# Kernel optimization log

Measured on AMD Instinct MI355X. Metric: run time of the kernel, lower is better.

## Reference

```python
import jax, jax.numpy as jnp
import numpy as np
import math

B, SQ, SK, D_MODEL, OUT_DIM = 8, 2048, 2048, 1024, 128
MASK_VALUE = -1e6  # torch code fills masked scores with -1000000.0, not -inf


def setup_inputs() -> dict:
    key = jax.random.key(0)
    ks = jax.random.split(key, 10)
    scale = 1.0 / math.sqrt(D_MODEL)
    return {
        "queries": jax.random.normal(ks[0], (B, SQ, D_MODEL), dtype=jnp.float32),
        "keys": jax.random.normal(ks[1], (B, SK, D_MODEL), dtype=jnp.float32),
        "values": jax.random.normal(ks[2], (B, SK, D_MODEL), dtype=jnp.float32),
        "valid_lens": jax.random.randint(ks[3], (B,), 1, SK + 1, dtype=jnp.int32),
        "w_q": jax.random.normal(ks[4], (D_MODEL, OUT_DIM), dtype=jnp.float32) * scale,
        "b_q": jnp.zeros((OUT_DIM,), dtype=jnp.float32),
        "w_k": jax.random.normal(ks[5], (D_MODEL, OUT_DIM), dtype=jnp.float32) * scale,
        "b_k": jnp.zeros((OUT_DIM,), dtype=jnp.float32),
        "w_v": jax.random.normal(ks[6], (D_MODEL, OUT_DIM), dtype=jnp.float32) * scale,
        "b_v": jnp.zeros((OUT_DIM,), dtype=jnp.float32),
    }


def reference(queries, keys, values, valid_lens, w_q, b_q, w_k, b_k, w_v, b_v):
    # QKV projections (LazyLinear equivalents)
    Q = queries @ w_q + b_q   # [B, SQ, OUT_DIM]
    K = keys @ w_k + b_k      # [B, SK, OUT_DIM]
    V = values @ w_v + b_v    # [B, SK, OUT_DIM]
    dim = Q.shape[-1]
    scores = jnp.einsum("bqd,bkd->bqk", Q, K) / jnp.sqrt(jnp.asarray(dim, Q.dtype))
    # masked_softmax: valid_lens [B] -> mask positions >= valid_len on the key axis
    mask = jnp.arange(scores.shape[-1])[None, None, :] < valid_lens[:, None, None]
    scores = jnp.where(mask, scores, jnp.asarray(MASK_VALUE, scores.dtype))
    attn = jax.nn.softmax(scores, axis=-1)
    return jnp.einsum("bqk,bkd->bqd", attn, V)  # [B, SQ, OUT_DIM]
```

## Files before the change

### kernel.cpp

```cpp
#include <hip/hip_runtime.h>
#include <math.h>

constexpr int BATCH  = 8;
constexpr int SEQQ   = 2048;
constexpr int SEQK   = 2048;
constexpr int DMODEL = 1024;
constexpr int ODIM   = 128;

typedef __attribute__((ext_vector_type(8))) short bf16x8;
typedef __attribute__((ext_vector_type(4))) float f32x4;

__device__ inline unsigned short f2bf(float f) {
    union { float f; unsigned int u; } v; v.f = f;
    unsigned int r = v.u + 0x7FFFu + ((v.u >> 16) & 1u);
    return (unsigned short)(r >> 16);
}

__device__ __forceinline__ unsigned int pk2bf(float a, float b) {
    unsigned int ua = __float_as_uint(a) + 0x8000u;
    unsigned int ub = __float_as_uint(b) + 0x8000u;
    return __builtin_amdgcn_perm(ub, ua, 0x07060302u);
}

__device__ __forceinline__ void gl_lds16(const void* g, void* l) {
    __builtin_amdgcn_global_load_lds(
        (const __attribute__((address_space(1))) unsigned int*)g,
        (__attribute__((address_space(3))) unsigned int*)l, 16, 0, 0);
}

__global__ __launch_bounds__(256)
void wtrans_kernel(const float* __restrict__ Wq, const float* __restrict__ Wk,
                   const float* __restrict__ Wv, unsigned short* __restrict__ Wt)
{
    const int which = blockIdx.z;
    const float* __restrict__ W = which == 0 ? Wq : (which == 1 ? Wk : Wv);
    unsigned short* __restrict__ dst = Wt + (size_t)which * DMODEL * ODIM;
    const int k0 = blockIdx.x * 32, n0 = blockIdx.y * 32;
    __shared__ unsigned short T[32][36];
    const int t = threadIdx.x;
    const int r = t >> 3, c = (t & 7) * 4;
    float4 w = *(const float4*)(W + (size_t)(k0 + r) * ODIM + n0 + c);
    T[r][c + 0] = f2bf(w.x); T[r][c + 1] = f2bf(w.y);
    T[r][c + 2] = f2bf(w.z); T[r][c + 3] = f2bf(w.w);
    __syncthreads();
    const int n = t >> 3, k4 = (t & 7) * 4;
    ushort4 o;
    o.x = T[k4 + 0][n]; o.y = T[k4 + 1][n];
    o.z = T[k4 + 2][n]; o.w = T[k4 + 3][n];
    *(ushort4*)(dst + (size_t)(n0 + n) * DMODEL + k0 + k4) = o;
}

__global__ __launch_bounds__(256, 6)
void proj_kernel(const float* __restrict__ Aq, const float* __restrict__ Ak,
                 const float* __restrict__ Av,
                 const unsigned short* __restrict__ Wt_all,
                 const float* __restrict__ bq, const float* __restrict__ bk,
                 const float* __restrict__ bv,
                 unsigned short* __restrict__ Qb, unsigned short* __restrict__ Kb,
                 unsigned short* __restrict__ Vt)
{
    const int which = blockIdx.y;
    const float* __restrict__ A    = which == 0 ? Aq : (which == 1 ? Ak : Av);
    const float* __restrict__ bias = which == 0 ? bq : (which == 1 ? bk : bv);
    const unsigned short* __restrict__ Wt = Wt_all + (size_t)which * DMODEL * ODIM;

    const int row0 = blockIdx.x * 32;
    const int t = threadIdx.x, wave = t >> 6, lane = t & 63;
    const int lrow = lane & 15, quad = lane >> 4;
    const int mh = (wave & 1) * 16;
    const int nh = (wave >> 1) * 64;

    __shared__ __align__(16) float          As[32 * 64];
    __shared__ __align__(16) unsigned short Ws[128 * 64];

    f32x4 acc[4];
#pragma unroll
    for (int nt = 0; nt < 4; ++nt)
#pragma unroll
        for (int i = 0; i < 4; ++i) acc[nt][i] = 0.f;

    const float* agp[2]; float* aldst[2];
    const unsigned short* wgp[4]; unsigned short* wldst[4];
#pragma unroll
    for (int j = 0; j < 2; ++j) {
        const int s = j * 256 + t;
        const int ar = s >> 4, ac = (s & 15) ^ (ar & 15);
        agp[j]   = A + (size_t)(row0 + ar) * DMODEL + ac * 4;
        aldst[j] = &As[s * 4];
    }
#pragma unroll
    for (int j = 0; j < 4; ++j) {
        const int s = j * 256 + t;
        const int wr = s >> 3, wc = (s & 7) ^ (wr & 7);
        wgp[j]   = Wt + (size_t)wr * DMODEL + wc * 8;
        wldst[j] = &Ws[s * 8];
    }

    const int R = mh + lrow;
    const int x4 = lrow;
    const int x3 = lrow & 7;

    for (int k0 = 0; k0 < DMODEL; k0 += 64) {
#pragma unroll
        for (int j = 0; j < 2; ++j) gl_lds16(agp[j] + k0, aldst[j]);
#pragma unroll
        for (int j = 0; j < 4; ++j) gl_lds16(wgp[j] + k0, wldst[j]);
        __syncthreads();
#pragma unroll
        for (int ks = 0; ks < 2; ++ks) {
            const int c0 = ks * 8 + quad * 2;
            float4 a0 = *(const float4*)&As[(R * 16 + (c0 ^ x4)) * 4];
            float4 a1 = *(const float4*)&As[(R * 16 + ((c0 + 1) ^ x4)) * 4];
            bf16x8 af;
            ((unsigned int*)&af)[0] = pk2bf(a0.x, a0.y);
            ((unsigned int*)&af)[1] = pk2bf(a0.z, a0.w);
            ((unsigned int*)&af)[2] = pk2bf(a1.x, a1.y);
            ((unsigned int*)&af)[3] = pk2bf(a1.z, a1.w);
#pragma unroll
            for (int nt = 0; nt < 4; ++nt) {
                const int n = nh + nt * 16 + lrow;
                const int c = (ks * 4 + quad) ^ x3;
                bf16x8 wf = *(const bf16x8*)&Ws[(n * 8 + c) * 8];
                acc[nt] = __builtin_amdgcn_mfma_f32_16x16x32_bf16(af, wf, acc[nt], 0, 0, 0);
            }
        }
        __syncthreads();
    }

    const float sc = (which == 0) ? 0.08838834764831845f : 1.0f;
    float bv_[4];
#pragma unroll
    for (int nt = 0; nt < 4; ++nt) bv_[nt] = bias[nh + nt * 16 + lrow];

    const int b  = row0 >> 11;
    const int mb = row0 & 2047;

    if (which == 2) {
#pragma unroll
        for (int nt = 0; nt < 4; ++nt) {
            const int n = nh + nt * 16 + lrow;
            ushort4 o;
            o.x = f2bf(acc[nt][0] + bv_[nt]);
            o.y = f2bf(acc[nt][1] + bv_[nt]);
            o.z = f2bf(acc[nt][2] + bv_[nt]);
            o.w = f2bf(acc[nt][3] + bv_[nt]);
            *(ushort4*)(Vt + ((size_t)b * ODIM + n) * SEQK + mb + mh + quad * 4) = o;
        }
    } else {
        unsigned short* __restrict__ Ob = (which == 0) ? Qb : Kb;
#pragma unroll
        for (int nt = 0; nt < 4; ++nt)
#pragma unroll
            for (int r = 0; r < 4; ++r) {
                float val = sc * (acc[nt][r] + bv_[nt]);
                Ob[(size_t)(row0 + mh + quad * 4 + r) * ODIM + nh + nt * 16 + lrow]
                    = f2bf(val);
            }
    }
}

__global__ __launch_bounds__(256, 3)
void flash_kernel(const unsigned short* __restrict__ Qb,
                  const unsigned short* __restrict__ Kb,
                  const unsigned short* __restrict__ Vt,
                  const int* __restrict__ valid_lens,
                  float* __restrict__ Op, float* __restrict__ Lp, int nsplit)
{
    const int b = blockIdx.y, s = blockIdx.z, q0 = blockIdx.x * 64;
    const int skh = SEQK / nsplit;
    const int t = threadIdx.x, wave = t >> 6, lane = t & 63;
    const int lrow = lane & 15, quad = lane >> 4;

    const int valid = valid_lens[b];
    const int vloc  = min(valid - s * skh, skh);

    float* __restrict__ lpart = Lp + (size_t)(s * BATCH + b) * SEQQ + q0;
    float* __restrict__ opart = Op + ((size_t)(s * BATCH + b) * SEQQ + q0) * ODIM;

    if (vloc <= 0) {
        if (t < 64) lpart[t] = 0.f;
        return;
    }

    __shared__ __align__(16) unsigned short Ks[64 * 128];
    __shared__ __align__(16) unsigned short Vs[128 * 64];
    __shared__ __align__(16) unsigned short Ps[4][16][72];

    bf16x8 qf[4];
    {
        const unsigned short* qp =
            Qb + ((size_t)b * SEQQ + q0 + wave * 16 + lrow) * ODIM + quad * 8;
#pragma unroll
        for (int ks = 0; ks < 4; ++ks) qf[ks] = *(const bf16x8*)(qp + ks * 32);
    }

    f32x4 o[8];
#pragma unroll
    for (int nt = 0; nt < 8; ++nt)
#pragma unroll
        for (int i = 0; i < 4; ++i) o[nt][i] = 0.f;
    float lsum[4] = {0.f, 0.f, 0.f, 0.f};

    const unsigned short* kgp[4]; unsigned short* kldst[4];
    const unsigned short* vgp[4]; unsigned short* vldst[4];
    const unsigned short* kbase = Kb + ((size_t)b * SEQK + s * skh) * ODIM;
    const unsigned short* vbase = Vt + (size_t)b * ODIM * SEQK + s * skh;
#pragma unroll
    for (int j = 0; j < 4; ++j) {
        const int sl = j * 256 + t;
        const int kr = sl >> 4, kc = (sl & 15) ^ (kr & 15);
        kgp[j]   = kbase + (size_t)kr * ODIM + kc * 8;
        kldst[j] = &Ks[sl * 8];
        const int vr = sl >> 3, vc = (sl & 7) ^ (vr & 7);
        vgp[j]   = vbase + (size_t)vr * SEQK + vc * 8;
        vldst[j] = &Vs[sl * 8];
    }

    const int x4 = lrow, x3 = lrow & 7;
    const int nch = (vloc + 63) >> 6;

    for (int c = 0; c < nch; ++c) {
        const int k0 = c * 64;
#pragma unroll
        for (int j = 0; j < 4; ++j) {
            gl_lds16(kgp[j] + (size_t)k0 * ODIM, kldst[j]);
            gl_lds16(vgp[j] + k0, vldst[j]);
        }
        __syncthreads();

        f32x4 sv[4];
#pragma unroll
        for (int nt = 0; nt < 4; ++nt)
#pragma unroll
            for (int i = 0; i < 4; ++i) sv[nt][i] = 0.f;
#pragma unroll
        for (int ks = 0; ks < 4; ++ks)
#pragma unroll
            for (int nt = 0; nt < 4; ++nt) {
                const int kr = nt * 16 + lrow;
                const int cc = (ks * 4 + quad) ^ x4;
                bf16x8 kf = *(const bf16x8*)&Ks[(kr * 16 + cc) * 8];
                sv[nt] = __builtin_amdgcn_mfma_f32_16x16x32_bf16(qf[ks], kf, sv[nt], 0, 0, 0);
            }

        if (k0 + 64 > vloc) {
#pragma unroll
            for (int nt = 0; nt < 4; ++nt)
                if (k0 + nt * 16 + lrow >= vloc) {
#pragma unroll
                    for (int i = 0; i < 4; ++i) sv[nt][i] = -1e30f;
                }
        }

#pragma unroll
        for (int nt = 0; nt < 4; ++nt)
#pragma unroll
            for (int r = 0; r < 4; ++r) {
                float p = __expf(sv[nt][r]);
                lsum[r] += p;
                Ps[wave][quad * 4 + r][nt * 16 + lrow] =
                    (unsigned short)((__float_as_uint(p) + 0x8000u) >> 16);
            }

        bf16x8 pf0 = *(const bf16x8*)&Ps[wave][lrow][quad * 8];
        bf16x8 pf1 = *(const bf16x8*)&Ps[wave][lrow][32 + quad * 8];

#pragma unroll
        for (int nt = 0; nt < 8; ++nt) {
            const int vrow = nt * 16 + lrow;
            bf16x8 v0 = *(const bf16x8*)&Vs[(vrow * 8 + (quad ^ x3)) * 8];
            o[nt] = __builtin_amdgcn_mfma_f32_16x16x32_bf16(pf0, v0, o[nt], 0, 0, 0);
        }
#pragma unroll
        for (int nt = 0; nt < 8; ++nt) {
            const int vrow = nt * 16 + lrow;
            bf16x8 v1 = *(const bf16x8*)&Vs[(vrow * 8 + ((4 + quad) ^ x3)) * 8];
            o[nt] = __builtin_amdgcn_mfma_f32_16x16x32_bf16(pf1, v1, o[nt], 0, 0, 0);
        }
        __syncthreads();
    }

#pragma unroll
    for (int msk = 1; msk < 16; msk <<= 1)
#pragma unroll
        for (int r = 0; r < 4; ++r) lsum[r] += __shfl_xor(lsum[r], msk);
    if (lrow == 0) {
#pragma unroll
        for (int r = 0; r < 4; ++r)
            lpart[wave * 16 + quad * 4 + r] = lsum[r];
    }

#pragma unroll
    for (int nt = 0; nt < 8; ++nt)
#pragma unroll
        for (int r = 0; r < 4; ++r)
            opart[(size_t)(wave * 16 + quad * 4 + r) * ODIM + nt * 16 + lrow]
                = o[nt][r];
}

__global__ __launch_bounds__(256)
void combine_kernel(const float* __restrict__ Op, const float* __restrict__ Lp,
                    float* __restrict__ out, int nsplit)
{
    const int idx = blockIdx.x * 256 + threadIdx.x;
    const int row = idx >> 5;
    const size_t SL = (size_t)BATCH * SEQQ;
    float l = 0.f;
    float4 acc = {0.f, 0.f, 0.f, 0.f};
    for (int s = 0; s < nsplit; ++s) {
        float ls = Lp[(size_t)s * SL + row];
        if (ls > 0.f) {
            float4 v = ((const float4*)(Op + (size_t)s * SL * ODIM))[idx];
            acc.x += v.x; acc.y += v.y; acc.z += v.z; acc.w += v.w;
            l += ls;
        }
    }
    const float inv = 1.f / l;
    float4 r;
    r.x = acc.x * inv; r.y = acc.y * inv; r.z = acc.z * inv; r.w = acc.w * inv;
    ((float4*)out)[idx] = r;
}

extern "C" void kernel_launch(void* const* d_in, const int* in_sizes, int n_in,
                              void* d_out, int out_size, void* d_ws, size_t ws_size,
                              hipStream_t stream)
{
    const float* queries    = (const float*)d_in[0];
    const float* keys       = (const float*)d_in[1];
    const float* values     = (const float*)d_in[2];
    const int*   valid_lens = (const int*)d_in[3];
    const float* w_q        = (const float*)d_in[4];
    const float* b_q        = (const float*)d_in[5];
    const float* w_k        = (const float*)d_in[6];
    const float* b_k        = (const float*)d_in[7];
    const float* w_v        = (const float*)d_in[8];
    const float* b_v        = (const float*)d_in[9];
    float* out = (float*)d_out;

    const size_t nQKV = (size_t)BATCH * SEQQ * ODIM;
    unsigned short* Qb = (unsigned short*)d_ws;
    unsigned short* Kb = Qb + nQKV;
    unsigned short* Vt = Kb + nQKV;
    unsigned short* Wt = Vt + nQKV;
    const size_t base = 3 * nQKV * sizeof(unsigned short)
                      + (size_t)3 * DMODEL * ODIM * sizeof(unsigned short);

    int KS = 4;
    if (ws_size < base + 4 * (nQKV * 4 + (size_t)BATCH * SEQQ * 4)) KS = 2;

    float* Op = (float*)((char*)d_ws + base);
    float* Lp = Op + (size_t)KS * nQKV;

    wtrans_kernel<<<dim3(DMODEL / 32, ODIM / 32, 3), 256, 0, stream>>>(w_q, w_k, w_v, Wt);

    proj_kernel<<<dim3((BATCH * SEQQ) / 32, 3), 256, 0, stream>>>(
        queries, keys, values, Wt, b_q, b_k, b_v, Qb, Kb, Vt);

    flash_kernel<<<dim3(SEQQ / 64, BATCH, KS), 256, 0, stream>>>(
        Qb, Kb, Vt, valid_lens, Op, Lp, KS);

    combine_kernel<<<(BATCH * SEQQ * ODIM / 4) / 256, 256, 0, stream>>>(Op, Lp, out, KS);
}
```

Baseline: 259.1 us.

## Double-buffer projection GEMM with register-staged A and larger row tile

The projection kernel now computes 64 rows per block instead of 32, with each wave owning a 32x64 output tile, so every W fragment read from LDS feeds two MFMAs. A is loaded into registers, converted to bf16 once and written to a swizzled bf16 LDS buffer. A and W are double-buffered so the next k-slice loads overlap the current MFMAs, which removes one barrier per iteration. This costs more LDS and registers: launch bounds drop to 3 blocks per SM and the grid is halved.

```diff
diff --git a/kernel.cpp b/kernel.cpp
--- a/kernel.cpp
+++ b/kernel.cpp
@@ -50,7 +50,7 @@
     *(ushort4*)(dst + (size_t)(n0 + n) * DMODEL + k0 + k4) = o;
 }
 
-__global__ __launch_bounds__(256, 6)
+__global__ __launch_bounds__(256, 3)
 void proj_kernel(const float* __restrict__ Aq, const float* __restrict__ Ak,
                  const float* __restrict__ Av,
                  const unsigned short* __restrict__ Wt_all,
@@ -64,98 +64,131 @@
     const float* __restrict__ bias = which == 0 ? bq : (which == 1 ? bk : bv);
     const unsigned short* __restrict__ Wt = Wt_all + (size_t)which * DMODEL * ODIM;
 
-    const int row0 = blockIdx.x * 32;
+    const int row0 = blockIdx.x * 64;
     const int t = threadIdx.x, wave = t >> 6, lane = t & 63;
     const int lrow = lane & 15, quad = lane >> 4;
-    const int mh = (wave & 1) * 16;
-    const int nh = (wave >> 1) * 64;
-
-    __shared__ __align__(16) float          As[32 * 64];
-    __shared__ __align__(16) unsigned short Ws[128 * 64];
-
-    f32x4 acc[4];
-#pragma unroll
-    for (int nt = 0; nt < 4; ++nt)
-#pragma unroll
-        for (int i = 0; i < 4; ++i) acc[nt][i] = 0.f;
-
-    const float* agp[2]; float* aldst[2];
-    const unsigned short* wgp[4]; unsigned short* wldst[4];
-#pragma unroll
-    for (int j = 0; j < 2; ++j) {
-        const int s = j * 256 + t;
-        const int ar = s >> 4, ac = (s & 15) ^ (ar & 15);
-        agp[j]   = A + (size_t)(row0 + ar) * DMODEL + ac * 4;
-        aldst[j] = &As[s * 4];
-    }
+    const int wrh = (wave & 1) * 32;
+    const int wch = (wave >> 1) * 64;
+
+    __shared__ __align__(16) unsigned short As[2][64 * 64];
+    __shared__ __align__(16) unsigned short Ws[2][128 * 64];
+
+    f32x4 acc[2][4];
+#pragma unroll
+    for (int mt = 0; mt < 2; ++mt)
+#pragma unroll
+        for (int nt = 0; nt < 4; ++nt)
+#pragma unroll
+            for (int i = 0; i < 4; ++i) acc[mt][nt][i] = 0.f;
+
+    const float* agp[4];
+    int awoff[4];
 #pragma unroll
     for (int j = 0; j < 4; ++j) {
         const int s = j * 256 + t;
-        const int wr = s >> 3, wc = (s & 7) ^ (wr & 7);
-        wgp[j]   = Wt + (size_t)wr * DMODEL + wc * 8;
-        wldst[j] = &Ws[s * 8];
-    }
-
-    const int R = mh + lrow;
-    const int x4 = lrow;
-    const int x3 = lrow & 7;
-
+        const int ar = s >> 4, ac = s & 15;
+        agp[j]   = A + (size_t)(row0 + ar) * DMODEL + ac * 4;
+        awoff[j] = ar * 64 + (((ac >> 1) ^ (ar & 7)) * 8) + (ac & 1) * 4;
+    }
+    const unsigned short* wgp[4];
+    int wloff[4];
+#pragma unroll
+    for (int j = 0; j < 4; ++j) {
+        const int s = j * 256 + t;
+        const int wr = s >> 3, wcc = (s & 7) ^ (wr & 7);
+        wgp[j]   = Wt + (size_t)wr * DMODEL + wcc * 8;
+        wloff[j] = s * 8;
+    }
+
+    const int x = lrow & 7;
+    float4 areg[4];
+
+#pragma unroll
+    for (int j = 0; j < 4; ++j) areg[j] = *(const float4*)(agp[j]);
+#pragma unroll
+    for (int j = 0; j < 4; ++j) gl_lds16(wgp[j], &Ws[0][wloff[j]]);
+#pragma unroll
+    for (int j = 0; j < 4; ++j) {
+        uint2 p;
+        p.x = pk2bf(areg[j].x, areg[j].y);
+        p.y = pk2bf(areg[j].z, areg[j].w);
+        *(uint2*)&As[0][awoff[j]] = p;
+    }
+    __syncthreads();
+
+    int cur = 0;
     for (int k0 = 0; k0 < DMODEL; k0 += 64) {
-#pragma unroll
-        for (int j = 0; j < 2; ++j) gl_lds16(agp[j] + k0, aldst[j]);
-#pragma unroll
-        for (int j = 0; j < 4; ++j) gl_lds16(wgp[j] + k0, wldst[j]);
+        const bool pf = (k0 + 64) < DMODEL;
+        if (pf) {
+#pragma unroll
+            for (int j = 0; j < 4; ++j)
+                areg[j] = *(const float4*)(agp[j] + k0 + 64);
+#pragma unroll
+            for (int j = 0; j < 4; ++j)
+                gl_lds16(wgp[j] + k0 + 64, &Ws[cur ^ 1][wloff[j]]);
+        }
+
+#pragma unroll
+        for (int ks = 0; ks < 2; ++ks) {
+            const int c = (ks * 4 + quad) ^ x;
+            bf16x8 af0 = *(const bf16x8*)&As[cur][(wrh + lrow) * 64 + c * 8];
+            bf16x8 af1 = *(const bf16x8*)&As[cur][(wrh + 16 + lrow) * 64 + c * 8];
+#pragma unroll
+            for (int nt = 0; nt < 4; ++nt) {
+                const int n = wch + nt * 16 + lrow;
+                bf16x8 wf = *(const bf16x8*)&Ws[cur][n * 64 + c * 8];
+                acc[0][nt] = __builtin_amdgcn_mfma_f32_16x16x32_bf16(af0, wf, acc[0][nt], 0, 0, 0);
+                acc[1][nt] = __builtin_amdgcn_mfma_f32_16x16x32_bf16(af1, wf, acc[1][nt], 0, 0, 0);
+            }
+        }
+
+        if (pf) {
+#pragma unroll
+            for (int j = 0; j < 4; ++j) {
+                uint2 p;
+                p.x = pk2bf(areg[j].x, areg[j].y);
+                p.y = pk2bf(areg[j].z, areg[j].w);
+                *(uint2*)&As[cur ^ 1][awoff[j]] = p;
+            }
+        }
         __syncthreads();
-#pragma unroll
-        for (int ks = 0; ks < 2; ++ks) {
-            const int c0 = ks * 8 + quad * 2;
-            float4 a0 = *(const float4*)&As[(R * 16 + (c0 ^ x4)) * 4];
-            float4 a1 = *(const float4*)&As[(R * 16 + ((c0 + 1) ^ x4)) * 4];
-            bf16x8 af;
-            ((unsigned int*)&af)[0] = pk2bf(a0.x, a0.y);
-            ((unsigned int*)&af)[1] = pk2bf(a0.z, a0.w);
-            ((unsigned int*)&af)[2] = pk2bf(a1.x, a1.y);
-            ((unsigned int*)&af)[3] = pk2bf(a1.z, a1.w);
-#pragma unroll
-            for (int nt = 0; nt < 4; ++nt) {
-                const int n = nh + nt * 16 + lrow;
-                const int c = (ks * 4 + quad) ^ x3;
-                bf16x8 wf = *(const bf16x8*)&Ws[(n * 8 + c) * 8];
-                acc[nt] = __builtin_amdgcn_mfma_f32_16x16x32_bf16(af, wf, acc[nt], 0, 0, 0);
-            }
-        }
-        __syncthreads();
+        cur ^= 1;
     }
 
     const float sc = (which == 0) ? 0.08838834764831845f : 1.0f;
     float bv_[4];
 #pragma unroll
-    for (int nt = 0; nt < 4; ++nt) bv_[nt] = bias[nh + nt * 16 + lrow];
+    for (int nt = 0; nt < 4; ++nt) bv_[nt] = bias[wch + nt * 16 + lrow];
 
     const int b  = row0 >> 11;
     const int mb = row0 & 2047;
 
     if (which == 2) {
 #pragma unroll
-        for (int nt = 0; nt < 4; ++nt) {
-            const int n = nh + nt * 16 + lrow;
-            ushort4 o;
-            o.x = f2bf(acc[nt][0] + bv_[nt]);
-            o.y = f2bf(acc[nt][1] + bv_[nt]);
-            o.z = f2bf(acc[nt][2] + bv_[nt]);
-            o.w = f2bf(acc[nt][3] + bv_[nt]);
-            *(ushort4*)(Vt + ((size_t)b * ODIM + n) * SEQK + mb + mh + quad * 4) = o;
-        }
+        for (int mt = 0; mt < 2; ++mt)
+#pragma unroll
+            for (int nt = 0; nt < 4; ++nt) {
+                const int n = wch + nt * 16 + lrow;
+                ushort4 o;
+                o.x = f2bf(acc[mt][nt][0] + bv_[nt]);
+                o.y = f2bf(acc[mt][nt][1] + bv_[nt]);
+                o.z = f2bf(acc[mt][nt][2] + bv_[nt]);
+                o.w = f2bf(acc[mt][nt][3] + bv_[nt]);
+                *(ushort4*)(Vt + ((size_t)b * ODIM + n) * SEQK
+                            + mb + wrh + mt * 16 + quad * 4) = o;
+            }
     } else {
         unsigned short* __restrict__ Ob = (which == 0) ? Qb : Kb;
 #pragma unroll
-        for (int nt = 0; nt < 4; ++nt)
-#pragma unroll
-            for (int r = 0; r < 4; ++r) {
-                float val = sc * (acc[nt][r] + bv_[nt]);
-                Ob[(size_t)(row0 + mh + quad * 4 + r) * ODIM + nh + nt * 16 + lrow]
-                    = f2bf(val);
-            }
+        for (int mt = 0; mt < 2; ++mt)
+#pragma unroll
+            for (int nt = 0; nt < 4; ++nt)
+#pragma unroll
+                for (int r = 0; r < 4; ++r) {
+                    float val = sc * (acc[mt][nt][r] + bv_[nt]);
+                    Ob[(size_t)(row0 + wrh + mt * 16 + quad * 4 + r) * ODIM
+                       + wch + nt * 16 + lrow] = f2bf(val);
+                }
     }
 }
 
@@ -353,7 +386,7 @@
 
     wtrans_kernel<<<dim3(DMODEL / 32, ODIM / 32, 3), 256, 0, stream>>>(w_q, w_k, w_v, Wt);
 
-    proj_kernel<<<dim3((BATCH * SEQQ) / 32, 3), 256, 0, stream>>>(
+    proj_kernel<<<dim3((BATCH * SEQQ) / 64, 3), 256, 0, stream>>>(
         queries, keys, values, Wt, b_q, b_k, b_v, Qb, Kb, Vt);
 
     flash_kernel<<<dim3(SEQQ / 64, BATCH, KS), 256, 0, stream>>>(
```

After: 262.4 us. No clear change (+1.2%).
